# Performance work log

Hardware: AMD Instinct MI355X
Metric: run time of the kernel (lower is better)

The kernel has to match this reference:

```python
import jax, jax.numpy as jnp
import numpy as np

BINS = 30
MOMENTUM = 0.75
LOSS_WEIGHT = 1.0


def setup_inputs() -> dict:
    key = jax.random.key(0)
    k1, k2 = jax.random.split(key)
    N, C = 8192, 2048
    preds = jax.random.normal(k1, (N, C), dtype=jnp.float32)
    targets = jax.random.randint(k2, (N, C), 0, 2).astype(jnp.int32)  # binary multi-hot
    acc_sum = jnp.zeros((BINS, C), dtype=jnp.float32)  # EMA histogram state
    return {"preds": preds, "targets": targets, "acc_sum": acc_sum}


def reference(preds, targets, acc_sum):
    N, C = preds.shape
    t = targets.astype(preds.dtype)

    # gradient norm g = |sigmoid(p) - t|, detached (weights carry no grad)
    g = jnp.abs(jax.nn.sigmoid(jax.lax.stop_gradient(preds)) - t)

    # bin index: edges[i] = i/BINS, so bin = floor(g*BINS), g=1.0 -> last bin (edge[-1]+=1e-6)
    bin_idx = jnp.clip(jnp.floor(g * BINS).astype(jnp.int32), 0, BINS - 1)  # [N, C]

    # per-label histogram: counts[b, c] = #examples with bin b in column c
    cols = jnp.broadcast_to(jnp.arange(C, dtype=jnp.int32)[None, :], (N, C))
    counts = jnp.zeros((BINS, C), dtype=preds.dtype).at[bin_idx, cols].add(1.0)

    # n[c] = number of non-empty bins for label c
    n = jnp.sum(counts >= 1.0, axis=0).astype(preds.dtype)  # [C]

    # EMA update of the histogram (momentum > 0 branch)
    acc_new = MOMENTUM * acc_sum + (1.0 - MOMENTUM) * counts  # [BINS, C]

    tot = jnp.asarray(float(max(N, 1.0)), preds.dtype)
    weights = tot / acc_new[bin_idx, cols]               # gather per-element density
    weights = weights / jnp.maximum(n, 1.0)[None, :]      # normalize by #valid bins
    weights = jax.lax.stop_gradient(weights)

    # BCE with logits, elementwise: softplus-style stable form
    bce = jnp.logaddexp(0.0, preds) - preds * t
    loss = jnp.mean(weights * bce)
    return loss * LOSS_WEIGHT
```

## Files before the change

### kernel.cpp

```cpp
#include <hip/hip_runtime.h>

#define BINS  30
#define NROWS 8192
#define NCOLS 2048
#define COLS_PER_BLK 256
#define ROWS_PER_BLK 128
#define YSLICES 64

#define FIXED_SCALE 16384.0f
#define CNT_SHIFT   24
#define SUM_MASK    ((1u << CNT_SHIFT) - 1)

#define WS_PART  0
#define WS_BPART (YSLICES * BINS * NCOLS * 4)
#define WS_CTR   (WS_BPART + 8 * 4)

__global__ __launch_bounds__(256, 5) void k_main(
    const float* __restrict__ preds, const int* __restrict__ targets,
    unsigned int* __restrict__ part, unsigned int* __restrict__ ctr)
{
    __shared__ unsigned int H[BINS * COLS_PER_BLK];
    const int t = threadIdx.x;
    if (blockIdx.x == 0 && blockIdx.y == 0 && t == 0) atomicExch(ctr, 0u);
    #pragma unroll
    for (int i = 0; i < BINS; ++i) H[i * COLS_PER_BLK + t] = 0u;
    __syncthreads();

    const int col = blockIdx.x * COLS_PER_BLK + t;
    const int r0  = blockIdx.y * ROWS_PER_BLK;
    const float* P = preds   + (size_t)r0 * NCOLS + col;
    const int*   T = targets + (size_t)r0 * NCOLS + col;

    float pc[8]; int tc[8];
    #pragma unroll
    for (int r = 0; r < 8; ++r) { pc[r] = P[r * NCOLS]; tc[r] = T[r * NCOLS]; }

    #pragma unroll 1
    for (int batch = 0; batch < ROWS_PER_BLK / 8; ++batch) {
        float pn[8]; int tn[8];
        if (batch < ROWS_PER_BLK / 8 - 1) {
            P += 8 * NCOLS; T += 8 * NCOLS;
            #pragma unroll
            for (int r = 0; r < 8; ++r) { pn[r] = P[r * NCOLS]; tn[r] = T[r * NCOLS]; }
        }
        __builtin_amdgcn_sched_barrier(0);

        #pragma unroll
        for (int r = 0; r < 8; ++r) {
            float p  = pc[r];
            float pp = tc[r] ? -p : p;
            float e  = __expf(-fabsf(pp));
            float d  = 1.0f + e;
            float r1 = __builtin_amdgcn_rcpf(d);
            float g  = (pp >= 0.0f) ? r1 : e * r1;
            int   b  = (int)(g * 30.0f);
            b = b > (BINS - 1) ? (BINS - 1) : b;
            float bce = fmaxf(pp, 0.0f) + __logf(d);
            unsigned int pk = (1u << CNT_SHIFT)
                | (unsigned int)(bce * FIXED_SCALE + 0.5f);
            H[b * COLS_PER_BLK + t] += pk;
        }
        #pragma unroll
        for (int r = 0; r < 8; ++r) { pc[r] = pn[r]; tc[r] = tn[r]; }
    }
    __syncthreads();

    const size_t outBase = (size_t)blockIdx.y * BINS * NCOLS
                         + (size_t)blockIdx.x * COLS_PER_BLK;
    for (int i = t; i < BINS * COLS_PER_BLK; i += 256)
        part[outBase + (size_t)(i >> 8) * NCOLS + (i & 255)] = H[i];
}

__global__ __launch_bounds__(512) void k_tail(
    const unsigned int* __restrict__ part,
    const float* __restrict__ acc_sum,
    float* __restrict__ blockPart, unsigned int* __restrict__ ctr,
    float* __restrict__ out)
{
    __shared__ unsigned int Lc[BINS * 256];
    __shared__ unsigned int Ls[BINS * 256];
    __shared__ float wave_sums[4];
    const int t  = threadIdx.x;
    const int cl = t & 255;
    const int q  = t >> 8;
    const int colBase = blockIdx.x * 256;

    unsigned int cq[BINS], sq[BINS];
    #pragma unroll
    for (int b = 0; b < BINS; ++b) { cq[b] = 0u; sq[b] = 0u; }

    const unsigned int* Pp = part + (size_t)(q * 32) * (BINS * NCOLS)
                                  + colBase + cl;
    #pragma unroll 1
    for (int y = 0; y < 32; ++y) {
        #pragma unroll
        for (int b = 0; b < BINS; ++b) {
            const unsigned int v = Pp[(size_t)b * NCOLS];
            cq[b] += v >> CNT_SHIFT;
            sq[b] += v & SUM_MASK;
        }
        Pp += BINS * NCOLS;
    }

    if (q == 1) {
        #pragma unroll
        for (int b = 0; b < BINS; ++b) {
            Lc[b * 256 + cl] = cq[b];
            Ls[b * 256 + cl] = sq[b];
        }
    }
    __syncthreads();

    if (q == 0) {
        const int c = colBase + cl;
        float colsum = 0.0f;
        int n = 0;
        #pragma unroll
        for (int b = 0; b < BINS; ++b) {
            const unsigned int cu = cq[b] + Lc[b * 256 + cl];
            const unsigned int su = sq[b] + Ls[b * 256 + cl];
            const float cnt = (float)cu;
            if (cnt >= 1.0f) {
                n += 1;
                float acc_new = 0.75f * acc_sum[(size_t)b * NCOLS + c] + 0.25f * cnt;
                colsum += ((float)su * (1.0f / FIXED_SCALE)) / acc_new;
            }
        }
        colsum /= (float)((n > 1 ? n : 1) * NCOLS);

        #pragma unroll
        for (int off = 32; off > 0; off >>= 1)
            colsum += __shfl_down(colsum, off, 64);
        if ((t & 63) == 0) wave_sums[t >> 6] = colsum;
    }
    __syncthreads();

    if (t == 0) {
        const float s = wave_sums[0] + wave_sums[1] + wave_sums[2] + wave_sums[3];
        atomicExch(&blockPart[blockIdx.x], s);
        __threadfence();
        if (atomicAdd(ctr, 1u) == 7u) {
            __threadfence();
            double d = 0.0;
            #pragma unroll
            for (int i = 0; i < 8; ++i)
                d += (double)atomicAdd(&blockPart[i], 0.0f);
            out[0] = (float)d;
        }
    }
}

extern "C" void kernel_launch(void* const* d_in, const int* in_sizes, int n_in,
                              void* d_out, int out_size, void* d_ws, size_t ws_size,
                              hipStream_t stream)
{
    const float* preds   = (const float*)d_in[0];
    const int*   targets = (const int*)d_in[1];
    const float* acc_sum = (const float*)d_in[2];

    unsigned int* part = (unsigned int*)((char*)d_ws + WS_PART);
    float* blockPart   = (float*)((char*)d_ws + WS_BPART);
    unsigned int* ctr  = (unsigned int*)((char*)d_ws + WS_CTR);

    dim3 gA(NCOLS / COLS_PER_BLK, NROWS / ROWS_PER_BLK);
    k_main<<<gA, 256, 0, stream>>>(preds, targets, part, ctr);

    k_tail<<<8, 512, 0, stream>>>(part, acc_sum, blockPart, ctr, (float*)d_out);
}
```

Baseline: 202.3 us.

## Split partial-histogram reduction into a wide parallel pre-reduce kernel

Adds a kernel with many threads that sums groups of 16 row-slice partial histograms and unpacks count and fixed-point sum in place. The final tail kernel then reads only four partials per cell instead of looping over 64 slices with few threads. This targets the latency-bound tail, which previously ran on only 8 blocks, at the cost of one extra kernel launch and an extra write/read pass.

```diff
diff --git a/kernel.cpp b/kernel.cpp
--- a/kernel.cpp
+++ b/kernel.cpp
@@ -6,6 +6,7 @@
 #define COLS_PER_BLK 256
 #define ROWS_PER_BLK 128
 #define YSLICES 64
+#define CELLS   (BINS * NCOLS)
 
 #define FIXED_SCALE 16384.0f
 #define CNT_SHIFT   24
@@ -71,68 +72,61 @@
         part[outBase + (size_t)(i >> 8) * NCOLS + (i & 255)] = H[i];
 }
 
-__global__ __launch_bounds__(512) void k_tail(
+__global__ __launch_bounds__(256) void k_reduce16(
+    unsigned int* __restrict__ part)
+{
+    const int gid   = blockIdx.x * 256 + threadIdx.x;
+    const int chunk = gid / CELLS;
+    const int cell  = gid % CELLS;
+    unsigned int* Pp = part + (size_t)(chunk * 16) * CELLS + cell;
+
+    unsigned int c = 0u, s = 0u;
+    #pragma unroll
+    for (int y = 0; y < 16; ++y) {
+        const unsigned int v = Pp[(size_t)y * CELLS];
+        c += v >> CNT_SHIFT;
+        s += v & SUM_MASK;
+    }
+    Pp[0]     = c;
+    Pp[CELLS] = s;
+}
+
+__global__ __launch_bounds__(256) void k_tail(
     const unsigned int* __restrict__ part,
     const float* __restrict__ acc_sum,
     float* __restrict__ blockPart, unsigned int* __restrict__ ctr,
     float* __restrict__ out)
 {
-    __shared__ unsigned int Lc[BINS * 256];
-    __shared__ unsigned int Ls[BINS * 256];
     __shared__ float wave_sums[4];
-    const int t  = threadIdx.x;
-    const int cl = t & 255;
-    const int q  = t >> 8;
-    const int colBase = blockIdx.x * 256;
+    const int t = threadIdx.x;
+    const int c = blockIdx.x * 256 + t;
 
-    unsigned int cq[BINS], sq[BINS];
+    float colsum = 0.0f;
+    int n = 0;
     #pragma unroll
-    for (int b = 0; b < BINS; ++b) { cq[b] = 0u; sq[b] = 0u; }
-
-    const unsigned int* Pp = part + (size_t)(q * 32) * (BINS * NCOLS)
-                                  + colBase + cl;
-    #pragma unroll 1
-    for (int y = 0; y < 32; ++y) {
-        #pragma unroll
-        for (int b = 0; b < BINS; ++b) {
-            const unsigned int v = Pp[(size_t)b * NCOLS];
-            cq[b] += v >> CNT_SHIFT;
-            sq[b] += v & SUM_MASK;
-        }
-        Pp += BINS * NCOLS;
-    }
-
-    if (q == 1) {
-        #pragma unroll
-        for (int b = 0; b < BINS; ++b) {
-            Lc[b * 256 + cl] = cq[b];
-            Ls[b * 256 + cl] = sq[b];
+    for (int b = 0; b < BINS; ++b) {
+        const int cell = b * NCOLS + c;
+        unsigned int cu = part[(size_t) 0 * CELLS + cell]
+                        + part[(size_t)16 * CELLS + cell]
+                        + part[(size_t)32 * CELLS + cell]
+                        + part[(size_t)48 * CELLS + cell];
+        unsigned int su = part[(size_t) 1 * CELLS + cell]
+                        + part[(size_t)17 * CELLS + cell]
+                        + part[(size_t)33 * CELLS + cell]
+                        + part[(size_t)49 * CELLS + cell];
+        const float cnt = (float)cu;
+        if (cnt >= 1.0f) {
+            n += 1;
+            float acc_new = 0.75f * acc_sum[cell] + 0.25f * cnt;
+            colsum += ((float)su * (1.0f / FIXED_SCALE)) / acc_new;
         }
     }
-    __syncthreads();
+    colsum /= (float)((n > 1 ? n : 1) * NCOLS);
 
-    if (q == 0) {
-        const int c = colBase + cl;
-        float colsum = 0.0f;
-        int n = 0;
-        #pragma unroll
-        for (int b = 0; b < BINS; ++b) {
-            const unsigned int cu = cq[b] + Lc[b * 256 + cl];
-            const unsigned int su = sq[b] + Ls[b * 256 + cl];
-            const float cnt = (float)cu;
-            if (cnt >= 1.0f) {
-                n += 1;
-                float acc_new = 0.75f * acc_sum[(size_t)b * NCOLS + c] + 0.25f * cnt;
-                colsum += ((float)su * (1.0f / FIXED_SCALE)) / acc_new;
-            }
-        }
-        colsum /= (float)((n > 1 ? n : 1) * NCOLS);
-
-        #pragma unroll
-        for (int off = 32; off > 0; off >>= 1)
-            colsum += __shfl_down(colsum, off, 64);
-        if ((t & 63) == 0) wave_sums[t >> 6] = colsum;
-    }
+    #pragma unroll
+    for (int off = 32; off > 0; off >>= 1)
+        colsum += __shfl_down(colsum, off, 64);
+    if ((t & 63) == 0) wave_sums[t >> 6] = colsum;
     __syncthreads();
 
     if (t == 0) {
@@ -165,5 +159,8 @@
     dim3 gA(NCOLS / COLS_PER_BLK, NROWS / ROWS_PER_BLK);
     k_main<<<gA, 256, 0, stream>>>(preds, targets, part, ctr);
 
-    k_tail<<<8, 512, 0, stream>>>(part, acc_sum, blockPart, ctr, (float*)d_out);
+    k_reduce16<<<(4 * CELLS) / 256, 256, 0, stream>>>(part);
+
+    k_tail<<<NCOLS / 256, 256, 0, stream>>>(part, acc_sum, blockPart, ctr,
+                                            (float*)d_out);
 }
```

New measurement: 180.0 us. 1.12x faster.
